# Optimization experiments

Hardware: AMD Instinct MI355X
Metric: run time of the kernel (lower is better)

The kernel has to match this reference:

```python
import jax, jax.numpy as jnp
import numpy as np

N_BATCHES = 32
N_LABELS = 100


def setup_inputs() -> dict:
    key = jax.random.key(0)
    ks = jax.random.split(key, 7)
    N, D, P = 16384, 2048, 256
    x = jax.random.normal(ks[0], (N, D), dtype=jnp.float32)
    label = jax.random.randint(ks[1], (N,), 0, N_LABELS, dtype=jnp.int64)
    label_batch = jnp.sort(jax.random.randint(ks[2], (N,), 0, N_BATCHES, dtype=jnp.int64))
    W1_w = jax.random.normal(ks[3], (P, D), dtype=jnp.float32) * 0.02
    W1_b = jax.random.normal(ks[4], (P,), dtype=jnp.float32) * 0.02
    W2_w = jax.random.normal(ks[5], (P, D), dtype=jnp.float32) * 0.02
    W2_b = jax.random.normal(ks[6], (P,), dtype=jnp.float32) * 0.02
    return {"x": x, "label": label, "label_batch": label_batch,
            "W1_w": W1_w, "W1_b": W1_b, "W2_w": W2_w, "W2_b": W2_b}


def _loo_diff_label_mean(x, label, label_batch):
    # For each sample i: mean of x over {j : label_batch[j]==label_batch[i] and label[j]!=label[i]}.
    # Rows with no such j are zero (torch code's `continue`). x is detached in the original.
    N = x.shape[0]
    xs = jax.lax.stop_gradient(x)
    seg = label_batch * N_LABELS + label                      # combined (group,label) key
    n_seg = N_BATCHES * N_LABELS
    ones = jnp.ones((N,), dtype=x.dtype)
    sum_bl = jax.ops.segment_sum(xs, seg, num_segments=n_seg)            # [n_seg, D]
    cnt_bl = jax.ops.segment_sum(ones, seg, num_segments=n_seg)          # [n_seg]
    sum_b = jax.ops.segment_sum(xs, label_batch, num_segments=N_BATCHES)  # [NB, D]
    cnt_b = jax.ops.segment_sum(ones, label_batch, num_segments=N_BATCHES)
    diff_sum = sum_b[label_batch] - sum_bl[seg]               # [N, D]
    diff_cnt = cnt_b[label_batch] - cnt_bl[seg]               # [N]
    safe = jnp.maximum(diff_cnt, 1.0)
    mean = diff_sum / safe[:, None]
    return jnp.where((diff_cnt > 0)[:, None], mean, jnp.zeros_like(mean))


def reference(x, label, label_batch, W1_w, W1_b, W2_w, W2_b):
    calc_mean = _loo_diff_label_mean(x, label, label_batch)   # detached aggregate
    return x @ W1_w.T + W1_b + calc_mean @ W2_w.T + W2_b      # W1(x) + W2(mean)
```

## Files before the change

### kernel.cpp

```cpp
#include <hip/hip_runtime.h>
#include <cstdint>

#define N_SAMPLES 16384
#define DIM 2048
#define PDIM 256
#define NB 32
#define NL 100
#define NSEG (NB * NL)

typedef float floatx4 __attribute__((ext_vector_type(4)));
typedef __bf16 bf16x8 __attribute__((ext_vector_type(8)));

__device__ __forceinline__ unsigned short f32_to_bf16(float f) {
    unsigned int u = __float_as_uint(f);
    u += 0x7fffu + ((u >> 16) & 1u);
    return (unsigned short)(u >> 16);
}
__device__ __forceinline__ unsigned int pack_bf16x2(float a, float b) {
    return (unsigned int)f32_to_bf16(a) | ((unsigned int)f32_to_bf16(b) << 16);
}

__global__ __launch_bounds__(256) void prep_kernel(
    const float* __restrict__ W1w, const float* __restrict__ W1b,
    const float* __restrict__ W2w, const float* __restrict__ W2b,
    const int* __restrict__ label, const int* __restrict__ lbatch,
    unsigned short* __restrict__ W1bf, unsigned short* __restrict__ W2bf,
    float* __restrict__ bias, int* __restrict__ seg,
    int* __restrict__ hist)
{
    int i = blockIdx.x * 256 + threadIdx.x;
    W1bf[i] = f32_to_bf16(W1w[i]);
    W2bf[i] = f32_to_bf16(W2w[i]);
    if (i < PDIM) bias[i] = W1b[i] + W2b[i];
    if (i < N_SAMPLES) seg[i] = lbatch[i] * NL + label[i];
    if (i < NSEG) hist[i] = 0;
}

__global__ __launch_bounds__(256) void hist_kernel(
    const int* __restrict__ seg, int* __restrict__ hist)
{
    int i = blockIdx.x * 256 + threadIdx.x;
    atomicAdd(&hist[seg[i]], 1);
}

#define SCAN_BPT 13
__global__ __launch_bounds__(256) void scan_kernel(
    const int* __restrict__ hist, int* __restrict__ offs, int* __restrict__ cursor)
{
    __shared__ int ps[256];
    const int t = threadIdx.x;
    int local = 0;
    #pragma unroll
    for (int k = 0; k < SCAN_BPT; ++k) {
        int bin = t * SCAN_BPT + k;
        if (bin < NSEG) local += hist[bin];
    }
    ps[t] = local;
    __syncthreads();
    for (int d = 1; d < 256; d <<= 1) {
        int v = (t >= d) ? ps[t - d] : 0;
        __syncthreads();
        ps[t] += v;
        __syncthreads();
    }
    int run = ps[t] - local;
    #pragma unroll
    for (int k = 0; k < SCAN_BPT; ++k) {
        int bin = t * SCAN_BPT + k;
        if (bin < NSEG) {
            offs[bin] = run;
            cursor[bin] = run;
            run += hist[bin];
        }
    }
    if (t == 255) offs[NSEG] = ps[255];
}

__global__ __launch_bounds__(256) void scatter_kernel(
    const int* __restrict__ seg, int* __restrict__ cursor, int* __restrict__ perm)
{
    int i = blockIdx.x * 256 + threadIdx.x;
    int pos = atomicAdd(&cursor[seg[i]], 1);
    perm[pos] = i;
}

__global__ __launch_bounds__(256) void segsum_kernel(
    const float* __restrict__ x, const int* __restrict__ perm,
    const int* __restrict__ offs,
    unsigned short* __restrict__ xb, float* __restrict__ sum_bl)
{
    const int tid = threadIdx.x;
    const int w = tid >> 6, lane = tid & 63;
    const int s = blockIdx.y * 4 + w;
    const int c = blockIdx.x * 512 + lane * 8;
    const int beg = offs[s], end = offs[s + 1];

    floatx4 sum0 = {0.f, 0.f, 0.f, 0.f};
    floatx4 sum1 = {0.f, 0.f, 0.f, 0.f};
    for (int base = beg; base < end; base += 64) {
        int p = (base + lane < end) ? perm[base + lane] : 0;
        const int n = min(end - base, 64);
        for (int j0 = 0; j0 < n; j0 += 4) {
            int rr[4];
            floatx4 v0[4], v1[4];
            #pragma unroll
            for (int j = 0; j < 4; ++j) {
                rr[j] = __shfl(p, min(j0 + j, n - 1));
                const float* px = &x[(size_t)rr[j] * DIM + c];
                v0[j] = *(const floatx4*)px;
                v1[j] = *(const floatx4*)(px + 4);
            }
            #pragma unroll
            for (int j = 0; j < 4; ++j) {
                if (j < n - j0) {
                    sum0 += v0[j];
                    sum1 += v1[j];
                    uint4 o;
                    o.x = pack_bf16x2(v0[j][0], v0[j][1]);
                    o.y = pack_bf16x2(v0[j][2], v0[j][3]);
                    o.z = pack_bf16x2(v1[j][0], v1[j][1]);
                    o.w = pack_bf16x2(v1[j][2], v1[j][3]);
                    *(uint4*)&xb[(size_t)rr[j] * DIM + c] = o;
                }
            }
        }
    }
    *(floatx4*)&sum_bl[(size_t)s * DIM + c] = sum0;
    *(floatx4*)&sum_bl[(size_t)s * DIM + c + 4] = sum1;
}

__global__ __launch_bounds__(256) void meanm_kernel(
    const float* __restrict__ sum_bl, const int* __restrict__ offs,
    unsigned short* __restrict__ Mb)
{
    __shared__ float acc[NL][256];
    const int tid = threadIdx.x;
    const int b = blockIdx.y;
    const int c = blockIdx.x * 256 + tid;

    float tot = 0.f;
    for (int l0 = 0; l0 < NL; l0 += 4) {
        float v[4];
        #pragma unroll
        for (int j = 0; j < 4; ++j)
            v[j] = sum_bl[(size_t)(b * NL + l0 + j) * DIM + c];
        #pragma unroll
        for (int j = 0; j < 4; ++j) { acc[l0 + j][tid] = v[j]; tot += v[j]; }
    }

    const int ob = offs[b * NL];
    const int cb = offs[(b + 1) * NL] - ob;
    for (int l = 0; l < NL; ++l) {
        int dc = cb - (offs[b * NL + l + 1] - offs[b * NL + l]);
        float m = (dc > 0) ? (tot - acc[l][tid]) / (float)dc : 0.f;
        Mb[(size_t)(b * NL + l) * DIM + c] = f32_to_bf16(m);
    }
}

template<int BM, int BN, bool FUSE>
__global__ __launch_bounds__(256) void gemm_bt_kernel(
    const unsigned short* __restrict__ A,
    const unsigned short* __restrict__ B,
    float* __restrict__ C,
    const float* __restrict__ bias,
    const float* __restrict__ add,
    const int* __restrict__ seg,
    int K)
{
    constexpr int HBM = BM / 2, HBN = BN / 2;
    constexpr int FM = BM / 32, FN = BN / 32;
    __shared__ __align__(16) unsigned short ldsA[BM * 32];
    __shared__ __align__(16) unsigned short ldsB[BN * 32];
    const int tid = threadIdx.x;
    const int lane = tid & 63;
    const int wave = tid >> 6;
    const int wr = wave >> 1, wc = wave & 1;
    const int quad = lane >> 4, l15 = lane & 15;
    const int m0 = blockIdx.x * BM;
    const int n0 = blockIdx.y * BN;
    const int srow = lane >> 2, schunk = lane & 3;

    floatx4 acc[FM][FN];
    #pragma unroll
    for (int i = 0; i < FM; ++i)
        #pragma unroll
        for (int j = 0; j < FN; ++j) acc[i][j] = (floatx4){0.f, 0.f, 0.f, 0.f};

    const unsigned short* Abase = A + (size_t)(m0 + srow) * K + schunk * 8;
    const unsigned short* Bbase = B + (size_t)(n0 + srow) * K + schunk * 8;

    for (int kk = 0; kk < K; kk += 32) {
        __syncthreads();
        #pragma unroll
        for (int ii = 0; ii < BM / 64; ++ii) {
            const int ch = ii * 4 + wave;
            __builtin_amdgcn_global_load_lds(
                (const __attribute__((address_space(1))) void*)(Abase + (size_t)ch * 16 * K + kk),
                (__attribute__((address_space(3))) void*)&ldsA[ch * 16 * 32], 16, 0, 0);
        }
        #pragma unroll
        for (int ii = 0; ii < BN / 64; ++ii) {
            const int ch = ii * 4 + wave;
            __builtin_amdgcn_global_load_lds(
                (const __attribute__((address_space(1))) void*)(Bbase + (size_t)ch * 16 * K + kk),
                (__attribute__((address_space(3))) void*)&ldsB[ch * 16 * 32], 16, 0, 0);
        }
        __syncthreads();

        bf16x8 af[FM], bfr[FN];
        #pragma unroll
        for (int mi = 0; mi < FM; ++mi)
            af[mi] = *(const bf16x8*)&ldsA[(wr * HBM + mi * 16 + l15) * 32 + quad * 8];
        #pragma unroll
        for (int ni = 0; ni < FN; ++ni)
            bfr[ni] = *(const bf16x8*)&ldsB[(wc * HBN + ni * 16 + l15) * 32 + quad * 8];
        #pragma unroll
        for (int mi = 0; mi < FM; ++mi)
            #pragma unroll
            for (int ni = 0; ni < FN; ++ni)
                acc[mi][ni] = __builtin_amdgcn_mfma_f32_16x16x32_bf16(
                    af[mi], bfr[ni], acc[mi][ni], 0, 0, 0);
    }

    #pragma unroll
    for (int mi = 0; mi < FM; ++mi) {
        const int rbase = m0 + wr * HBM + mi * 16 + quad * 4;
        #pragma unroll
        for (int ni = 0; ni < FN; ++ni) {
            const int col = n0 + wc * HBN + ni * 16 + l15;
            float bsum = 0.f;
            if constexpr (FUSE) bsum = bias[col];
            #pragma unroll
            for (int r = 0; r < 4; ++r) {
                const int row = rbase + r;
                float v = acc[mi][ni][r];
                if constexpr (FUSE) v += bsum + add[(size_t)seg[row] * PDIM + col];
                C[(size_t)row * PDIM + col] = v;
            }
        }
    }
}

extern "C" void kernel_launch(void* const* d_in, const int* in_sizes, int n_in,
                              void* d_out, int out_size, void* d_ws, size_t ws_size,
                              hipStream_t stream)
{
    const float* x      = (const float*)d_in[0];
    const int*   label  = (const int*)d_in[1];
    const int*   lbatch = (const int*)d_in[2];
    const float* W1w    = (const float*)d_in[3];
    const float* W1b    = (const float*)d_in[4];
    const float* W2w    = (const float*)d_in[5];
    const float* W2b    = (const float*)d_in[6];
    float* out = (float*)d_out;

    char* ws = (char*)d_ws;
    size_t off = 0;
    auto alloc = [&](size_t bytes) {
        void* p = ws + off;
        off = (off + bytes + 255) & ~(size_t)255;
        return p;
    };
    unsigned short* xb   = (unsigned short*)alloc((size_t)N_SAMPLES * DIM * 2);
    unsigned short* Mb   = (unsigned short*)alloc((size_t)NSEG * DIM * 2);
    unsigned short* W1bf = (unsigned short*)alloc((size_t)PDIM * DIM * 2);
    unsigned short* W2bf = (unsigned short*)alloc((size_t)PDIM * DIM * 2);
    float* MW2    = (float*)alloc((size_t)NSEG * PDIM * 4);
    float* sum_bl = (float*)alloc((size_t)NSEG * DIM * 4);
    float* bias   = (float*)alloc(PDIM * 4);
    int*   seg    = (int*)alloc(N_SAMPLES * 4);
    int*   perm   = (int*)alloc(N_SAMPLES * 4);
    int*   hist   = (int*)alloc(NSEG * 4);
    int*   offs   = (int*)alloc((NSEG + 1) * 4);
    int*   cursor = (int*)alloc(NSEG * 4);

    prep_kernel<<<PDIM * DIM / 256, 256, 0, stream>>>(
        W1w, W1b, W2w, W2b, label, lbatch, W1bf, W2bf, bias, seg, hist);

    hist_kernel<<<N_SAMPLES / 256, 256, 0, stream>>>(seg, hist);
    scan_kernel<<<1, 256, 0, stream>>>(hist, offs, cursor);
    scatter_kernel<<<N_SAMPLES / 256, 256, 0, stream>>>(seg, cursor, perm);

    segsum_kernel<<<dim3(DIM / 512, NSEG / 4), 256, 0, stream>>>(
        x, perm, offs, xb, sum_bl);

    meanm_kernel<<<dim3(DIM / 256, NB), 256, 0, stream>>>(sum_bl, offs, Mb);

    gemm_bt_kernel<64, 64, false><<<dim3(NSEG / 64, PDIM / 64), 256, 0, stream>>>(
        Mb, W2bf, MW2, nullptr, nullptr, nullptr, DIM);

    gemm_bt_kernel<128, 64, true><<<dim3(N_SAMPLES / 128, PDIM / 64), 256, 0, stream>>>(
        xb, W1bf, out, bias, MW2, seg, DIM);
}
```

Measured before the change: 325.2 us.

## Generalize GEMM wave layout, add split-K for mean GEMM, deepen segsum unroll

The GEMM kernel now takes a configurable wave layout and a split-K factor. The small mean-times-W2 GEMM runs with 32x256 tiles split over two K halves and accumulated with atomics, so MW2 is zeroed in the prep kernel. The main GEMM switches from 128x64 to 64x128 tiles. The segment-sum loop now keeps eight rows of loads in flight instead of four. These changes aim to improve occupancy and memory-level parallelism, at the cost of atomic traffic and more register pressure.

```diff
diff --git a/kernel.cpp b/kernel.cpp
--- a/kernel.cpp
+++ b/kernel.cpp
@@ -26,7 +26,7 @@
     const int* __restrict__ label, const int* __restrict__ lbatch,
     unsigned short* __restrict__ W1bf, unsigned short* __restrict__ W2bf,
     float* __restrict__ bias, int* __restrict__ seg,
-    int* __restrict__ hist)
+    int* __restrict__ hist, float* __restrict__ MW2)
 {
     int i = blockIdx.x * 256 + threadIdx.x;
     W1bf[i] = f32_to_bf16(W1w[i]);
@@ -34,6 +34,7 @@
     if (i < PDIM) bias[i] = W1b[i] + W2b[i];
     if (i < N_SAMPLES) seg[i] = lbatch[i] * NL + label[i];
     if (i < NSEG) hist[i] = 0;
+    if (i < NSEG * PDIM / 2) ((float2*)MW2)[i] = make_float2(0.f, 0.f);
 }
 
 __global__ __launch_bounds__(256) void hist_kernel(
@@ -100,18 +101,18 @@
     for (int base = beg; base < end; base += 64) {
         int p = (base + lane < end) ? perm[base + lane] : 0;
         const int n = min(end - base, 64);
-        for (int j0 = 0; j0 < n; j0 += 4) {
-            int rr[4];
-            floatx4 v0[4], v1[4];
-            #pragma unroll
-            for (int j = 0; j < 4; ++j) {
+        for (int j0 = 0; j0 < n; j0 += 8) {
+            int rr[8];
+            floatx4 v0[8], v1[8];
+            #pragma unroll
+            for (int j = 0; j < 8; ++j) {
                 rr[j] = __shfl(p, min(j0 + j, n - 1));
                 const float* px = &x[(size_t)rr[j] * DIM + c];
                 v0[j] = *(const floatx4*)px;
                 v1[j] = *(const floatx4*)(px + 4);
             }
             #pragma unroll
-            for (int j = 0; j < 4; ++j) {
+            for (int j = 0; j < 8; ++j) {
                 if (j < n - j0) {
                     sum0 += v0[j];
                     sum1 += v1[j];
@@ -157,7 +158,7 @@
     }
 }
 
-template<int BM, int BN, bool FUSE>
+template<int BM, int BN, int WR, int WC, bool FUSE, int KSPLIT>
 __global__ __launch_bounds__(256) void gemm_bt_kernel(
     const unsigned short* __restrict__ A,
     const unsigned short* __restrict__ B,
@@ -167,17 +168,19 @@
     const int* __restrict__ seg,
     int K)
 {
-    constexpr int HBM = BM / 2, HBN = BN / 2;
-    constexpr int FM = BM / 32, FN = BN / 32;
+    constexpr int SM = BM / WR, SN = BN / WC;
+    constexpr int FM = SM / 16, FN = SN / 16;
     __shared__ __align__(16) unsigned short ldsA[BM * 32];
     __shared__ __align__(16) unsigned short ldsB[BN * 32];
     const int tid = threadIdx.x;
     const int lane = tid & 63;
     const int wave = tid >> 6;
-    const int wr = wave >> 1, wc = wave & 1;
+    const int wr = wave / WC, wc = wave % WC;
     const int quad = lane >> 4, l15 = lane & 15;
     const int m0 = blockIdx.x * BM;
     const int n0 = blockIdx.y * BN;
+    const int kpw = K / KSPLIT;
+    const int k0 = blockIdx.z * kpw;
     const int srow = lane >> 2, schunk = lane & 3;
 
     floatx4 acc[FM][FN];
@@ -189,31 +192,27 @@
     const unsigned short* Abase = A + (size_t)(m0 + srow) * K + schunk * 8;
     const unsigned short* Bbase = B + (size_t)(n0 + srow) * K + schunk * 8;
 
-    for (int kk = 0; kk < K; kk += 32) {
-        __syncthreads();
-        #pragma unroll
-        for (int ii = 0; ii < BM / 64; ++ii) {
-            const int ch = ii * 4 + wave;
+    for (int kk = k0; kk < k0 + kpw; kk += 32) {
+        __syncthreads();
+        #pragma unroll
+        for (int ch = wave; ch < BM / 16; ch += 4)
             __builtin_amdgcn_global_load_lds(
                 (const __attribute__((address_space(1))) void*)(Abase + (size_t)ch * 16 * K + kk),
                 (__attribute__((address_space(3))) void*)&ldsA[ch * 16 * 32], 16, 0, 0);
-        }
-        #pragma unroll
-        for (int ii = 0; ii < BN / 64; ++ii) {
-            const int ch = ii * 4 + wave;
+        #pragma unroll
+        for (int ch = wave; ch < BN / 16; ch += 4)
             __builtin_amdgcn_global_load_lds(
                 (const __attribute__((address_space(1))) void*)(Bbase + (size_t)ch * 16 * K + kk),
                 (__attribute__((address_space(3))) void*)&ldsB[ch * 16 * 32], 16, 0, 0);
-        }
         __syncthreads();
 
         bf16x8 af[FM], bfr[FN];
         #pragma unroll
         for (int mi = 0; mi < FM; ++mi)
-            af[mi] = *(const bf16x8*)&ldsA[(wr * HBM + mi * 16 + l15) * 32 + quad * 8];
+            af[mi] = *(const bf16x8*)&ldsA[(wr * SM + mi * 16 + l15) * 32 + quad * 8];
         #pragma unroll
         for (int ni = 0; ni < FN; ++ni)
-            bfr[ni] = *(const bf16x8*)&ldsB[(wc * HBN + ni * 16 + l15) * 32 + quad * 8];
+            bfr[ni] = *(const bf16x8*)&ldsB[(wc * SN + ni * 16 + l15) * 32 + quad * 8];
         #pragma unroll
         for (int mi = 0; mi < FM; ++mi)
             #pragma unroll
@@ -224,10 +223,10 @@
 
     #pragma unroll
     for (int mi = 0; mi < FM; ++mi) {
-        const int rbase = m0 + wr * HBM + mi * 16 + quad * 4;
+        const int rbase = m0 + wr * SM + mi * 16 + quad * 4;
         #pragma unroll
         for (int ni = 0; ni < FN; ++ni) {
-            const int col = n0 + wc * HBN + ni * 16 + l15;
+            const int col = n0 + wc * SN + ni * 16 + l15;
             float bsum = 0.f;
             if constexpr (FUSE) bsum = bias[col];
             #pragma unroll
@@ -235,7 +234,10 @@
                 const int row = rbase + r;
                 float v = acc[mi][ni][r];
                 if constexpr (FUSE) v += bsum + add[(size_t)seg[row] * PDIM + col];
-                C[(size_t)row * PDIM + col] = v;
+                if constexpr (KSPLIT > 1)
+                    atomicAdd(&C[(size_t)row * PDIM + col], v);
+                else
+                    C[(size_t)row * PDIM + col] = v;
             }
         }
     }
@@ -275,7 +277,7 @@
     int*   cursor = (int*)alloc(NSEG * 4);
 
     prep_kernel<<<PDIM * DIM / 256, 256, 0, stream>>>(
-        W1w, W1b, W2w, W2b, label, lbatch, W1bf, W2bf, bias, seg, hist);
+        W1w, W1b, W2w, W2b, label, lbatch, W1bf, W2bf, bias, seg, hist, MW2);
 
     hist_kernel<<<N_SAMPLES / 256, 256, 0, stream>>>(seg, hist);
     scan_kernel<<<1, 256, 0, stream>>>(hist, offs, cursor);
@@ -286,9 +288,11 @@
 
     meanm_kernel<<<dim3(DIM / 256, NB), 256, 0, stream>>>(sum_bl, offs, Mb);
 
-    gemm_bt_kernel<64, 64, false><<<dim3(NSEG / 64, PDIM / 64), 256, 0, stream>>>(
+    gemm_bt_kernel<32, 256, 1, 4, false, 2>
+        <<<dim3(NSEG / 32, 1, 2), 256, 0, stream>>>(
         Mb, W2bf, MW2, nullptr, nullptr, nullptr, DIM);
 
-    gemm_bt_kernel<128, 64, true><<<dim3(N_SAMPLES / 128, PDIM / 64), 256, 0, stream>>>(
+    gemm_bt_kernel<64, 128, 2, 2, true, 1>
+        <<<dim3(N_SAMPLES / 64, PDIM / 128), 256, 0, stream>>>(
         xb, W1bf, out, bias, MW2, seg, DIM);
 }
```

Result: faster. 317.7 us (-2.3%).
